# Kernel tuning notes

Hardware: AMD Instinct MI355X
Metric: run time of the kernel (lower is better)

## Reference

```python
import jax, jax.numpy as jnp
import numpy as np

N_QUBITS = 10
DIM = 2 ** N_QUBITS  # 1024

# PennyLane QFT (wire 0 = MSB): QFT|x> = (1/sqrt(N)) sum_y exp(2*pi*i*x*y/N)|y>
_idx = np.arange(DIM)
QFT_MAT = jnp.asarray(np.exp(2j * np.pi * np.outer(_idx, _idx) / DIM) / np.sqrt(DIM), dtype=jnp.complex64)


def _rx(t):
    c = jnp.cos(0.5 * t).astype(jnp.complex64)
    s = jnp.sin(0.5 * t).astype(jnp.complex64)
    return jnp.stack([jnp.stack([c, -1j * s]), jnp.stack([-1j * s, c])])


def _ry(t):
    c = jnp.cos(0.5 * t).astype(jnp.complex64)
    s = jnp.sin(0.5 * t).astype(jnp.complex64)
    return jnp.stack([jnp.stack([c, -s]), jnp.stack([s, c])])


def _rz(t):
    e = jnp.exp(-0.5j * t.astype(jnp.complex64))
    z = jnp.zeros((), jnp.complex64)
    return jnp.stack([jnp.stack([e, z]), jnp.stack([z, jnp.conj(e)])])


def _apply_1q(state, U, q):
    # state: (B,) + (2,)*N_QUBITS; contract qubit axis q+1 with 2x2 gate U
    s = jnp.tensordot(U, state, axes=[[1], [q + 1]])  # new qubit axis moves to front
    return jnp.moveaxis(s, 0, q + 1)


def _apply_cnot(state, c, t):
    # flip target-qubit axis on the control=1 slice
    s0 = jax.lax.index_in_dim(state, 0, c + 1, keepdims=True)
    s1 = jax.lax.index_in_dim(state, 1, c + 1, keepdims=True)
    s1 = jnp.flip(s1, axis=t + 1)
    return jnp.concatenate([s0, s1], axis=c + 1)


def _forward(x, weights):
    B = x.shape[0]
    pad = DIM - x.shape[-1]
    xp = jnp.pad(x, ((0, 0), (0, pad))) if pad > 0 else x[..., :DIM]
    nrm = jnp.maximum(jnp.linalg.norm(xp, axis=-1, keepdims=True), 1e-8)
    state = (xp / nrm).astype(jnp.complex64).reshape((B,) + (2,) * N_QUBITS)

    for q in range(N_QUBITS):
        state = _apply_1q(state, _rx(weights[q, 0]), q)
    for q in range(N_QUBITS):
        state = _apply_1q(state, _ry(weights[q, 1]), q)
    for q in range(N_QUBITS):
        state = _apply_1q(state, _rz(weights[q, 2]), q)
    for q in range(N_QUBITS):  # ring entanglement
        state = _apply_cnot(state, q, (q + 1) % N_QUBITS)
    for q in range(N_QUBITS):
        state = _apply_1q(state, _ry(weights[q, 3]), q)

    # QFT over all wires as one dense matmul on the flattened statevector
    state = (state.reshape(B, DIM) @ QFT_MAT.T).reshape((B,) + (2,) * N_QUBITS)

    ex, ey, ez = [], [], []
    for q in range(N_QUBITS):
        a = jax.lax.index_in_dim(state, 0, q + 1, keepdims=False)
        b = jax.lax.index_in_dim(state, 1, q + 1, keepdims=False)
        axes = tuple(range(1, a.ndim))
        zab = jnp.sum(jnp.conj(a) * b, axis=axes)  # (B,)
        ex.append(2.0 * jnp.real(zab))             # <X_q>
        ey.append(2.0 * jnp.imag(zab))             # <Y_q>
        ez.append(jnp.sum(jnp.real(jnp.conj(a) * a - jnp.conj(b) * b), axis=axes))  # <Z_q>
    return jnp.stack(ex + ey + ez, axis=1).astype(jnp.float32)  # (B, 3*N_QUBITS)


def setup_inputs() -> dict:
    key = jax.random.key(0)
    k1, k2 = jax.random.split(key)
    x = jax.random.normal(k1, (8192, 768), dtype=jnp.float32)
    weights = jax.random.normal(k2, (N_QUBITS, 4), dtype=jnp.float32) * 0.01
    return {"x": x, "weights": weights}


def reference(x, weights):
    return _forward(x, weights)
```

## Files before the change

### kernel.cpp

```cpp
#include <hip/hip_runtime.h>
#include <math.h>

#define NFEAT 768
#define NT    256

typedef float f2 __attribute__((ext_vector_type(2)));

__device__ __forceinline__ int swz(int j){ return j ^ (j >> 4) ^ ((j >> 2) & 0xC); }

__device__ __forceinline__ int cnot_perm(int j){
  int i = j;
  i ^= ((i >> 0) & 1) << 9;
  i ^= ((i >> 1) & 1) << 0;
  i ^= ((i >> 2) & 1) << 1;
  i ^= ((i >> 3) & 1) << 2;
  i ^= ((i >> 4) & 1) << 3;
  i ^= ((i >> 5) & 1) << 4;
  i ^= ((i >> 6) & 1) << 5;
  i ^= ((i >> 7) & 1) << 6;
  i ^= ((i >> 8) & 1) << 7;
  i ^= ((i >> 9) & 1) << 8;
  return i;
}

template<int CTRL>
__device__ __forceinline__ float dpp_mov(float x){
  return __builtin_bit_cast(float,
    __builtin_amdgcn_update_dpp(0, __builtin_bit_cast(int, x), CTRL, 0xF, 0xF, true));
}
template<int CTRL>
__device__ __forceinline__ float dpp_add(float x){ return x + dpp_mov<CTRL>(x); }

__device__ __forceinline__ f2 pk_cmul(f2 s, f2 v){
  f2 d;
  asm("v_pk_mul_f32 %0, %1, %2 op_sel:[0,0] op_sel_hi:[0,1]\n\t"
      "v_pk_fma_f32 %0, %1, %2, %0 op_sel:[1,1,0] op_sel_hi:[1,0,1] neg_lo:[0,1,0]"
      : "=&v"(d) : "v"(s), "v"(v));
  return d;
}
__device__ __forceinline__ f2 pk_cfma(f2 s, f2 v, f2 acc){
  f2 d;
  asm("v_pk_fma_f32 %0, %2, %3, %1 op_sel:[0,0,0] op_sel_hi:[0,1,1]\n\t"
      "v_pk_fma_f32 %0, %2, %3, %0 op_sel:[1,1,0] op_sel_hi:[1,0,1] neg_lo:[0,1,0]"
      : "=&v"(d) : "v"(acc), "v"(s), "v"(v));
  return d;
}
__device__ __forceinline__ f2 pk_cross(f2 a, f2 b, f2 acc){
  f2 d;
  asm("v_pk_fma_f32 %0, %2, %3, %1 op_sel:[0,1,0] op_sel_hi:[1,0,1] neg_hi:[1,0,0]"
      : "=&v"(d) : "v"(acc), "v"(a), "v"(b));
  return d;
}
__device__ __forceinline__ void pk_ry(f2 cs, f2& a, f2& b){
  f2 t1, t2, na, nb;
  asm("v_pk_mul_f32 %0, %2, %3 op_sel:[1,0] op_sel_hi:[1,1] neg_lo:[1,0] neg_hi:[1,0]\n\t"
      "v_pk_mul_f32 %1, %2, %4 op_sel:[1,0] op_sel_hi:[1,1]"
      : "=&v"(t1), "=&v"(t2) : "v"(cs), "v"(b), "v"(a));
  asm("v_pk_fma_f32 %0, %2, %3, %4 op_sel:[0,0,0] op_sel_hi:[0,1,1]\n\t"
      "v_pk_fma_f32 %1, %2, %5, %6 op_sel:[0,0,0] op_sel_hi:[0,1,1]"
      : "=&v"(na), "=&v"(nb) : "v"(cs), "v"(a), "v"(t1), "v"(b), "v"(t2));
  a = na; b = nb;
}
__device__ __forceinline__ void gateU(const f2* g, f2& a, f2& b){
  const f2 na = pk_cfma(g[1], b, pk_cmul(g[0], a));
  const f2 nb = pk_cfma(g[3], b, pk_cmul(g[2], a));
  a = na; b = nb;
}
__device__ __forceinline__ void bfly(f2& a, f2& b, f2 tw){
  const f2 u = a + b, v = a - b;
  a = u; b = pk_cmul(tw, v);
}
__device__ __forceinline__ void bfly1(f2& a, f2& b){
  const f2 u = a + b, v = a - b; a = u; b = v;
}
__device__ __forceinline__ void bflyI(f2& a, f2& b){
  const f2 u = a + b, v = a - b; a = u; b = f2{-v.y, v.x};
}

template<int MASK>
__device__ __forceinline__ void gate_on(f2* xv, const f2* g){
  #pragma unroll
  for (int m = 0; m < 16; ++m) if (!(m & MASK)) gateU(g, xv[m], xv[m|MASK]);
}
template<int MASK>
__device__ __forceinline__ void ry_on(f2* xv, const f2 cs){
  #pragma unroll
  for (int m = 0; m < 16; ++m) if (!(m & MASK)) pk_ry(cs, xv[m], xv[m|MASK]);
}

template<int SH>
__device__ __forceinline__ void rd16(const f2* bb, int a0, f2* xv){
  #pragma unroll
  for (int m = 0; m < 16; ++m) xv[m] = bb[a0 ^ swz(m << SH)];
}
template<int SH>
__device__ __forceinline__ void wr16(f2* bb, int a0, const f2* xv){
  #pragma unroll
  for (int m = 0; m < 16; ++m) bb[a0 ^ swz(m << SH)] = xv[m];
}

__device__ __forceinline__ void fft16(f2* xv, const f2 BT){
  const f2 T64c  = { 0.9238795325112867f, 0.3826834323650898f };
  const f2 T128c = { 0.7071067811865476f, 0.7071067811865476f };
  const f2 tB = pk_cmul(BT, BT);
  const f2 tC = pk_cmul(tB, tB);
  const f2 tD = pk_cmul(tC, tC);
  { f2 tw = BT;
    bfly(xv[0], xv[8], tw);
    #pragma unroll
    for (int m = 1; m < 8; ++m){ tw = pk_cmul(tw, T64c); bfly(xv[m], xv[m+8], tw); } }
  { f2 tw = tB;
    bfly(xv[0], xv[4], tw); bfly(xv[8], xv[12], tw);
    #pragma unroll
    for (int k = 1; k < 4; ++k){ tw = pk_cmul(tw, T128c); bfly(xv[k], xv[k+4], tw); bfly(xv[8+k], xv[12+k], tw); } }
  { const f2 itC = {-tC.y, tC.x};
    #pragma unroll
    for (int m = 0; m < 16; ++m) if (!(m & 2)) bfly(xv[m], xv[m|2], (m & 1) ? itC : tC); }
  #pragma unroll
  for (int m = 0; m < 16; m += 2) bfly(xv[m], xv[m+1], tD);
}

template<int MASK>
__device__ __forceinline__ f2 pairsum16(const f2* z){
  f2 rp = {0.f, 0.f}, ip = {0.f, 0.f};
  #pragma unroll
  for (int m = 0; m < 16; ++m) if (!(m & MASK)){
    rp = z[m]*z[m|MASK] + rp;
    ip = pk_cross(z[m], z[m|MASK], ip);
  }
  return f2{ rp.x + rp.y, ip.x + ip.y };
}

__global__ void gate_prep(const float* __restrict__ w, float* __restrict__ gt){
  const int t = threadIdx.x;
  if (t >= 10) return;
  const float ha = 0.5f*w[t*4+0], hb = 0.5f*w[t*4+1];
  const float hg = 0.5f*w[t*4+2], hd = 0.5f*w[t*4+3];
  const float ca = cosf(ha), sa = sinf(ha);
  const float cb = cosf(hb), sb = sinf(hb);
  const float cg = cosf(hg), sg = sinf(hg);
  const float m00r = cb*ca, m00i =  sb*sa;
  const float m01r = -sb*ca, m01i = -cb*sa;
  const float m10r =  sb*ca, m10i = -cb*sa;
  const float m11r = cb*ca,  m11i = -sb*sa;
  gt[8*t+0] = cg*m00r + sg*m00i;  gt[8*t+1] = cg*m00i - sg*m00r;
  gt[8*t+2] = cg*m01r + sg*m01i;  gt[8*t+3] = cg*m01i - sg*m01r;
  gt[8*t+4] = cg*m10r - sg*m10i;  gt[8*t+5] = cg*m10i + sg*m10r;
  gt[8*t+6] = cg*m11r - sg*m11i;  gt[8*t+7] = cg*m11i + sg*m11r;
  gt[80+2*t] = cosf(hd); gt[81+2*t] = sinf(hd);
}

__global__ void __launch_bounds__(NT)
qqk_kernel(const float* __restrict__ x, const float* __restrict__ gt,
           float* __restrict__ out)
{
  __shared__ f2 smem[4*1024];
  const int t = threadIdx.x, wave = t >> 6, lane = t & 63;
  f2* bb = smem + (wave << 10);
  const f2* g2  = (const f2*)gt;
  const f2* gry = (const f2*)(gt + 80);
  const size_t e = (size_t)blockIdx.x * 4 + wave;
  const float* xg = x + e * NFEAT;

  const int aA = swz(lane);
  const int aB = swz(((lane >> 2) << 6) | (lane & 3));
  const int aC = swz(lane << 4);

  f2 xv[16];
  float ss = 0.f;
  #pragma unroll
  for (int m = 0; m < 12; ++m){ const float v = xg[(m << 6) + lane]; xv[m] = f2{v, 0.f}; ss += v*v; }
  #pragma unroll
  for (int m = 12; m < 16; ++m) xv[m] = f2{0.f, 0.f};
  ss = dpp_add<0xB1>(ss); ss = dpp_add<0x4E>(ss);
  ss += __shfl_xor(ss, 4); ss += __shfl_xor(ss, 8); ss += __shfl_xor(ss, 16); ss += __shfl_xor(ss, 32);
  const float invn = 1.0f / fmaxf(sqrtf(ss), 1e-8f);
  #pragma unroll
  for (int m = 0; m < 12; ++m) xv[m].x *= invn;
  gate_on<8>(xv, g2+0); gate_on<4>(xv, g2+4); gate_on<2>(xv, g2+8); gate_on<1>(xv, g2+12);
  wr16<6>(bb, aA, xv);
  rd16<2>(bb, aB, xv);
  gate_on<8>(xv, g2+16); gate_on<4>(xv, g2+20); gate_on<2>(xv, g2+24); gate_on<1>(xv, g2+28);
  wr16<2>(bb, aB, xv);
  rd16<0>(bb, aC, xv);
  gate_on<2>(xv, g2+32); gate_on<1>(xv, g2+36);
  wr16<0>(bb, aC, xv);
  { const int ag = swz(cnot_perm(lane));
    #pragma unroll
    for (int m = 0; m < 16; ++m) xv[m] = bb[ag ^ swz(cnot_perm(m << 6))];
  }
  ry_on<8>(xv, gry[0]); ry_on<4>(xv, gry[1]); ry_on<2>(xv, gry[2]); ry_on<1>(xv, gry[3]);
  wr16<6>(bb, aA, xv);
  rd16<2>(bb, aB, xv);
  ry_on<8>(xv, gry[4]); ry_on<4>(xv, gry[5]); ry_on<2>(xv, gry[6]); ry_on<1>(xv, gry[7]);
  wr16<2>(bb, aB, xv);
  rd16<0>(bb, aC, xv);
  ry_on<2>(xv, gry[8]); ry_on<1>(xv, gry[9]);
  wr16<0>(bb, aC, xv);
  rd16<6>(bb, aA, xv);
  { float sa, ca; __sincosf((float)lane * 6.135923151542565e-3f, &sa, &ca);
    fft16(xv, f2{ca, sa}); }
  wr16<6>(bb, aA, xv);
  rd16<2>(bb, aB, xv);
  { float sa, ca; __sincosf((float)(lane & 3) * 9.817477042468104e-2f, &sa, &ca);
    fft16(xv, f2{ca, sa}); }
  wr16<2>(bb, aB, xv);
  rd16<0>(bb, aC, xv);
  #pragma unroll
  for (int m = 0; m < 16; ++m) if (!(m & 2)){ if (m & 1) bflyI(xv[m], xv[m|2]); else bfly1(xv[m], xv[m|2]); }
  #pragma unroll
  for (int m = 0; m < 16; m += 2) bfly1(xv[m], xv[m+1]);
  wr16<0>(bb, aC, xv);
  f2 xrxi[10];
  xrxi[0] = pairsum16<1>(xv); xrxi[1] = pairsum16<2>(xv);
  xrxi[2] = pairsum16<4>(xv); xrxi[3] = pairsum16<8>(xv);
  float S = 0.f, z0 = 0.f, z1 = 0.f, z2 = 0.f, z3 = 0.f;
  #pragma unroll
  for (int m = 0; m < 16; ++m){
    const f2 q = xv[m]*xv[m]; const float n = q.x + q.y;
    S += n;
    z0 += (m & 1) ? -n : n;  z1 += (m & 2) ? -n : n;
    z2 += (m & 4) ? -n : n;  z3 += (m & 8) ? -n : n;
  }
  rd16<6>(bb, aA, xv);
  xrxi[6] = pairsum16<1>(xv); xrxi[7] = pairsum16<2>(xv);
  xrxi[8] = pairsum16<4>(xv); xrxi[9] = pairsum16<8>(xv);
  rd16<2>(bb, aB, xv);
  xrxi[4] = pairsum16<4>(xv); xrxi[5] = pairsum16<8>(xv);

  float d0, d1, d2, d3, d4, d5;
  { float s = S, wv;
    wv = dpp_mov<0xB1>(s); d0 = (lane & 1)  ? (wv - s) : (s - wv); s += wv;
    wv = dpp_mov<0x4E>(s); d1 = (lane & 2)  ? (wv - s) : (s - wv); s += wv;
    wv = __shfl_xor(s, 4);  d2 = (lane & 4)  ? (wv - s) : (s - wv); s += wv;
    wv = __shfl_xor(s, 8);  d3 = (lane & 8)  ? (wv - s) : (s - wv); s += wv;
    wv = __shfl_xor(s, 16); d4 = (lane & 16) ? (wv - s) : (s - wv); s += wv;
    wv = __shfl_xor(s, 32); d5 = (lane & 32) ? (wv - s) : (s - wv); s += wv;
    d0 = dpp_add<0x4E>(d0); d0 += __shfl_xor(d0, 4); d0 += __shfl_xor(d0, 8); d0 += __shfl_xor(d0, 16); d0 += __shfl_xor(d0, 32);
    d1 += __shfl_xor(d1, 4); d1 += __shfl_xor(d1, 8); d1 += __shfl_xor(d1, 16); d1 += __shfl_xor(d1, 32);
    d2 += __shfl_xor(d2, 8); d2 += __shfl_xor(d2, 16); d2 += __shfl_xor(d2, 32);
    d3 += __shfl_xor(d3, 16); d3 += __shfl_xor(d3, 32);
    d4 += __shfl_xor(d4, 32);
  }

  #pragma unroll
  for (int q = 0; q < 10; ++q){
    xrxi[q].x = dpp_add<0x4E>(dpp_add<0xB1>(xrxi[q].x));
    xrxi[q].y = dpp_add<0x4E>(dpp_add<0xB1>(xrxi[q].y));
  }
  z0 = dpp_add<0x4E>(dpp_add<0xB1>(z0));
  z1 = dpp_add<0x4E>(dpp_add<0xB1>(z1));
  z2 = dpp_add<0x4E>(dpp_add<0xB1>(z2));
  z3 = dpp_add<0x4E>(dpp_add<0xB1>(z3));
  float* rb = (float*)bb;
  const int g = lane >> 2;
  if ((lane & 3) == 0){
    #pragma unroll
    for (int q = 0; q < 10; ++q){ rb[q*16 + g] = xrxi[q].x; rb[(10+q)*16 + g] = xrxi[q].y; }
    rb[20*16 + g] = z0; rb[21*16 + g] = z1; rb[22*16 + g] = z2; rb[23*16 + g] = z3;
  }
  float* ob = out + e * 30;
  if (lane < 24){
    float acc = 0.f;
    #pragma unroll
    for (int gg = 0; gg < 16; ++gg) acc += rb[lane*16 + gg];
    ob[lane] = acc * ((lane < 20) ? (2.0f/1024.0f) : (1.0f/1024.0f));
  }
  if (lane == 0){
    const float zs = 1.0f/1024.0f;
    ob[24] = d0*zs; ob[25] = d1*zs; ob[26] = d2*zs;
    ob[27] = d3*zs; ob[28] = d4*zs; ob[29] = d5*zs;
  }
}

extern "C" void kernel_launch(void* const* d_in, const int* in_sizes, int n_in,
                              void* d_out, int out_size, void* d_ws, size_t ws_size,
                              hipStream_t stream) {
  const float* x = (const float*)d_in[0];
  const float* w = (const float*)d_in[1];
  float* out = (float*)d_out;
  float* gt  = (float*)d_ws;
  const int B = in_sizes[0] / NFEAT;
  gate_prep<<<1, 16, 0, stream>>>(w, gt);
  qqk_kernel<<<B/4, NT, 0, stream>>>(x, gt, out);
}
```

Baseline: 47.53 us.

## Remap statevector LDS layout for 128-bit vectorized shared-memory transposes

Reassigns qubits so that each lane holds adjacent amplitude pairs, which lets every LDS transpose use float4 loads and stores instead of scalar f2 accesses, with a new XOR swizzle. The global input load also becomes float2. The gate schedule and FFT stages are rewritten for the new mapping: one 8-point radix split per stage with precomputed twiddle constants. Compiler memory fences are added between shared-memory phases, and the new layout risks bank conflicts or indexing errors.

New measurement: 45.61 us. 4.0% less time.

```diff
diff --git a/kernel.cpp b/kernel.cpp
--- a/kernel.cpp
+++ b/kernel.cpp
@@ -5,8 +5,9 @@
 #define NT    256
 
 typedef float f2 __attribute__((ext_vector_type(2)));
-
-__device__ __forceinline__ int swz(int j){ return j ^ (j >> 4) ^ ((j >> 2) & 0xC); }
+#define MEMFENCE() asm volatile("" ::: "memory")
+
+__device__ __forceinline__ int swz2(int j){ return j ^ ((j >> 3) & 0xE); }
 
 __device__ __forceinline__ int cnot_perm(int j){
   int i = j;
@@ -66,6 +67,7 @@
   const f2 nb = pk_cfma(g[3], b, pk_cmul(g[2], a));
   a = na; b = nb;
 }
+__device__ __forceinline__ f2 rot90(f2 v){ return f2{-v.y, v.x}; }
 __device__ __forceinline__ void bfly(f2& a, f2& b, f2 tw){
   const f2 u = a + b, v = a - b;
   a = u; b = pk_cmul(tw, v);
@@ -87,39 +89,6 @@
   #pragma unroll
   for (int m = 0; m < 16; ++m) if (!(m & MASK)) pk_ry(cs, xv[m], xv[m|MASK]);
 }
-
-template<int SH>
-__device__ __forceinline__ void rd16(const f2* bb, int a0, f2* xv){
-  #pragma unroll
-  for (int m = 0; m < 16; ++m) xv[m] = bb[a0 ^ swz(m << SH)];
-}
-template<int SH>
-__device__ __forceinline__ void wr16(f2* bb, int a0, const f2* xv){
-  #pragma unroll
-  for (int m = 0; m < 16; ++m) bb[a0 ^ swz(m << SH)] = xv[m];
-}
-
-__device__ __forceinline__ void fft16(f2* xv, const f2 BT){
-  const f2 T64c  = { 0.9238795325112867f, 0.3826834323650898f };
-  const f2 T128c = { 0.7071067811865476f, 0.7071067811865476f };
-  const f2 tB = pk_cmul(BT, BT);
-  const f2 tC = pk_cmul(tB, tB);
-  const f2 tD = pk_cmul(tC, tC);
-  { f2 tw = BT;
-    bfly(xv[0], xv[8], tw);
-    #pragma unroll
-    for (int m = 1; m < 8; ++m){ tw = pk_cmul(tw, T64c); bfly(xv[m], xv[m+8], tw); } }
-  { f2 tw = tB;
-    bfly(xv[0], xv[4], tw); bfly(xv[8], xv[12], tw);
-    #pragma unroll
-    for (int k = 1; k < 4; ++k){ tw = pk_cmul(tw, T128c); bfly(xv[k], xv[k+4], tw); bfly(xv[8+k], xv[12+k], tw); } }
-  { const f2 itC = {-tC.y, tC.x};
-    #pragma unroll
-    for (int m = 0; m < 16; ++m) if (!(m & 2)) bfly(xv[m], xv[m|2], (m & 1) ? itC : tC); }
-  #pragma unroll
-  for (int m = 0; m < 16; m += 2) bfly(xv[m], xv[m+1], tD);
-}
-
 template<int MASK>
 __device__ __forceinline__ f2 pairsum16(const f2* z){
   f2 rp = {0.f, 0.f}, ip = {0.f, 0.f};
@@ -129,6 +98,43 @@
     ip = pk_cross(z[m], z[m|MASK], ip);
   }
   return f2{ rp.x + rp.y, ip.x + ip.y };
+}
+
+__device__ __forceinline__ void rdA(const f2* bb, int a0, f2* xv){
+  #pragma unroll
+  for (int k = 0; k < 8; ++k){
+    const float4 v = *(const float4*)(bb + (a0 ^ (k << 7)));
+    xv[2*k] = f2{v.x, v.y}; xv[2*k+1] = f2{v.z, v.w};
+  }
+}
+__device__ __forceinline__ void wrA(f2* bb, int a0, const f2* xv){
+  #pragma unroll
+  for (int k = 0; k < 8; ++k)
+    *(float4*)(bb + (a0 ^ (k << 7))) = make_float4(xv[2*k].x, xv[2*k].y, xv[2*k+1].x, xv[2*k+1].y);
+}
+__device__ __forceinline__ void rdB(const f2* bb, int a0, f2* xv){
+  #pragma unroll
+  for (int k = 0; k < 8; ++k){
+    const float4 v = *(const float4*)(bb + (a0 ^ ((k << 4) | (k << 1))));
+    xv[2*k] = f2{v.x, v.y}; xv[2*k+1] = f2{v.z, v.w};
+  }
+}
+__device__ __forceinline__ void wrB(f2* bb, int a0, const f2* xv){
+  #pragma unroll
+  for (int k = 0; k < 8; ++k)
+    *(float4*)(bb + (a0 ^ ((k << 4) | (k << 1)))) = make_float4(xv[2*k].x, xv[2*k].y, xv[2*k+1].x, xv[2*k+1].y);
+}
+__device__ __forceinline__ void rdC(const f2* bb, int a0, f2* xv){
+  #pragma unroll
+  for (int k = 0; k < 8; ++k){
+    const float4 v = *(const float4*)(bb + (a0 ^ (k << 1)));
+    xv[2*k] = f2{v.x, v.y}; xv[2*k+1] = f2{v.z, v.w};
+  }
+}
+__device__ __forceinline__ void wrC(f2* bb, int a0, const f2* xv){
+  #pragma unroll
+  for (int k = 0; k < 8; ++k)
+    *(float4*)(bb + (a0 ^ (k << 1))) = make_float4(xv[2*k].x, xv[2*k].y, xv[2*k+1].x, xv[2*k+1].y);
 }
 
 __global__ void gate_prep(const float* __restrict__ w, float* __restrict__ gt){
@@ -154,7 +160,7 @@
 qqk_kernel(const float* __restrict__ x, const float* __restrict__ gt,
            float* __restrict__ out)
 {
-  __shared__ f2 smem[4*1024];
+  __shared__ __align__(16) f2 smem[4096];
   const int t = threadIdx.x, wave = t >> 6, lane = t & 63;
   f2* bb = smem + (wave << 10);
   const f2* g2  = (const f2*)gt;
@@ -162,14 +168,28 @@
   const size_t e = (size_t)blockIdx.x * 4 + wave;
   const float* xg = x + e * NFEAT;
 
-  const int aA = swz(lane);
-  const int aB = swz(((lane >> 2) << 6) | (lane & 3));
-  const int aC = swz(lane << 4);
+  const int aA = (lane << 1) ^ ((lane >> 2) & 14);
+  const int aB = ((lane >> 3) << 7) | ((lane & 7) << 1);
+  const int aC = (lane << 4) ^ ((lane << 1) & 14);
+
+  const f2 T1c   = { 0.9999811752826011f, 0.0061358846491545f };
+  const f2 T2c   = { 0.9999247018391445f, 0.0122715382857199f };
+  const f2 T4c   = { 0.9996988186962042f, 0.0245412285229123f };
+  const f2 T8c   = { 0.9987954562051724f, 0.0490676743274180f };
+  const f2 T16c  = { 0.9951847266721969f, 0.0980171403295606f };
+  const f2 T32c  = { 0.9807852804032304f, 0.1950903220161283f };
+  const float c45 = 0.7071067811865476f, c22 = 0.9238795325112867f, s22 = 0.3826834323650898f;
+  const f2 T64c  = { c22, s22 };
+  const f2 T128c = { c45, c45 };
 
   f2 xv[16];
   float ss = 0.f;
   #pragma unroll
-  for (int m = 0; m < 12; ++m){ const float v = xg[(m << 6) + lane]; xv[m] = f2{v, 0.f}; ss += v*v; }
+  for (int k = 0; k < 6; ++k){
+    const float2 v = *(const float2*)(xg + (k << 7) + (lane << 1));
+    xv[2*k] = f2{v.x, 0.f}; xv[2*k+1] = f2{v.y, 0.f};
+    ss += v.x*v.x + v.y*v.y;
+  }
   #pragma unroll
   for (int m = 12; m < 16; ++m) xv[m] = f2{0.f, 0.f};
   ss = dpp_add<0xB1>(ss); ss = dpp_add<0x4E>(ss);
@@ -177,40 +197,98 @@
   const float invn = 1.0f / fmaxf(sqrtf(ss), 1e-8f);
   #pragma unroll
   for (int m = 0; m < 12; ++m) xv[m].x *= invn;
-  gate_on<8>(xv, g2+0); gate_on<4>(xv, g2+4); gate_on<2>(xv, g2+8); gate_on<1>(xv, g2+12);
-  wr16<6>(bb, aA, xv);
-  rd16<2>(bb, aB, xv);
-  gate_on<8>(xv, g2+16); gate_on<4>(xv, g2+20); gate_on<2>(xv, g2+24); gate_on<1>(xv, g2+28);
-  wr16<2>(bb, aB, xv);
-  rd16<0>(bb, aC, xv);
-  gate_on<2>(xv, g2+32); gate_on<1>(xv, g2+36);
-  wr16<0>(bb, aC, xv);
-  { const int ag = swz(cnot_perm(lane));
-    #pragma unroll
-    for (int m = 0; m < 16; ++m) xv[m] = bb[ag ^ swz(cnot_perm(m << 6))];
-  }
-  ry_on<8>(xv, gry[0]); ry_on<4>(xv, gry[1]); ry_on<2>(xv, gry[2]); ry_on<1>(xv, gry[3]);
-  wr16<6>(bb, aA, xv);
-  rd16<2>(bb, aB, xv);
-  ry_on<8>(xv, gry[4]); ry_on<4>(xv, gry[5]); ry_on<2>(xv, gry[6]); ry_on<1>(xv, gry[7]);
-  wr16<2>(bb, aB, xv);
-  rd16<0>(bb, aC, xv);
-  ry_on<2>(xv, gry[8]); ry_on<1>(xv, gry[9]);
-  wr16<0>(bb, aC, xv);
-  rd16<6>(bb, aA, xv);
-  { float sa, ca; __sincosf((float)lane * 6.135923151542565e-3f, &sa, &ca);
-    fft16(xv, f2{ca, sa}); }
-  wr16<6>(bb, aA, xv);
-  rd16<2>(bb, aB, xv);
-  { float sa, ca; __sincosf((float)(lane & 3) * 9.817477042468104e-2f, &sa, &ca);
-    fft16(xv, f2{ca, sa}); }
-  wr16<2>(bb, aB, xv);
-  rd16<0>(bb, aC, xv);
-  #pragma unroll
-  for (int m = 0; m < 16; ++m) if (!(m & 2)){ if (m & 1) bflyI(xv[m], xv[m|2]); else bfly1(xv[m], xv[m|2]); }
+  gate_on<8>(xv, g2+0); gate_on<4>(xv, g2+4); gate_on<2>(xv, g2+8); gate_on<1>(xv, g2+36);
+  wrA(bb, aA, xv);
+  MEMFENCE();
+  rdB(bb, aB, xv);
+  gate_on<8>(xv, g2+12); gate_on<4>(xv, g2+16); gate_on<2>(xv, g2+20);
+  wrB(bb, aB, xv);
+  MEMFENCE();
+  rdC(bb, aC, xv);
+  gate_on<8>(xv, g2+24); gate_on<4>(xv, g2+28); gate_on<2>(xv, g2+32);
+  wrC(bb, aC, xv);
+  MEMFENCE();
+  { const int ag = swz2(cnot_perm(lane << 4));
+    #pragma unroll
+    for (int m = 0; m < 16; ++m) xv[m] = bb[ag ^ swz2(cnot_perm(m))];
+  }
+  MEMFENCE();
+  ry_on<8>(xv, gry[6]); ry_on<4>(xv, gry[7]); ry_on<2>(xv, gry[8]); ry_on<1>(xv, gry[9]);
+  wrC(bb, aC, xv);
+  MEMFENCE();
+  rdB(bb, aB, xv);
+  ry_on<8>(xv, gry[3]); ry_on<4>(xv, gry[4]); ry_on<2>(xv, gry[5]);
+  wrB(bb, aB, xv);
+  MEMFENCE();
+  rdA(bb, aA, xv);
+  ry_on<8>(xv, gry[0]); ry_on<4>(xv, gry[1]); ry_on<2>(xv, gry[2]);
+  { float sa, ca; __sincosf((float)lane * 1.2271846303085130e-2f, &sa, &ca);
+    const f2 BT = {ca, sa};
+    const f2 BT2 = pk_cmul(BT, BT);
+    const f2 BT4 = pk_cmul(BT2, BT2);
+    f2 t9[8];
+    t9[0] = BT;               t9[1] = pk_cmul(BT, T1c);
+    t9[2] = pk_cmul(BT, T128c); t9[3] = pk_cmul(t9[1], T128c);
+    t9[4] = rot90(t9[0]); t9[5] = rot90(t9[1]); t9[6] = rot90(t9[2]); t9[7] = rot90(t9[3]);
+    #pragma unroll
+    for (int m = 0; m < 8; ++m) bfly(xv[m], xv[m+8], t9[m]);
+    f2 u[4];
+    u[0] = BT2; u[1] = pk_cmul(BT2, T2c); u[2] = rot90(u[0]); u[3] = rot90(u[1]);
+    #pragma unroll
+    for (int m = 0; m < 16; ++m) if (!(m & 4)) bfly(xv[m], xv[m|4], u[m & 3]);
+    f2 v2[2];
+    v2[0] = BT4; v2[1] = pk_cmul(BT4, T4c);
+    #pragma unroll
+    for (int m = 0; m < 16; ++m) if (!(m & 2)) bfly(xv[m], xv[m|2], v2[m & 1]);
+  }
+  wrA(bb, aA, xv);
+  MEMFENCE();
+  rdB(bb, aB, xv);
+  { float sa, ca; __sincosf((float)(lane & 7) * 9.8174770424681035e-2f, &sa, &ca);
+    const f2 CT = {ca, sa};
+    const f2 CT2 = pk_cmul(CT, CT);
+    const f2 CT4 = pk_cmul(CT2, CT2);
+    f2 t6[8];
+    t6[0] = CT;               t6[1] = pk_cmul(CT, T8c);
+    t6[2] = pk_cmul(CT, T128c); t6[3] = pk_cmul(t6[1], T128c);
+    t6[4] = rot90(t6[0]); t6[5] = rot90(t6[1]); t6[6] = rot90(t6[2]); t6[7] = rot90(t6[3]);
+    #pragma unroll
+    for (int m = 0; m < 8; ++m) bfly(xv[m], xv[m+8], t6[m]);
+    f2 u[4];
+    u[0] = CT2; u[1] = pk_cmul(CT2, T16c); u[2] = rot90(u[0]); u[3] = rot90(u[1]);
+    #pragma unroll
+    for (int m = 0; m < 16; ++m) if (!(m & 4)) bfly(xv[m], xv[m|4], u[m & 3]);
+    f2 v2[2];
+    v2[0] = CT4; v2[1] = pk_cmul(CT4, T32c);
+    #pragma unroll
+    for (int m = 0; m < 16; ++m) if (!(m & 2)) bfly(xv[m], xv[m|2], v2[m & 1]);
+  }
+  wrB(bb, aB, xv);
+  MEMFENCE();
+  rdC(bb, aC, xv);
+  bfly1(xv[0], xv[8]);
+  bfly (xv[1], xv[9],  T64c);
+  bfly (xv[2], xv[10], T128c);
+  bfly (xv[3], xv[11], f2{ s22, c22});
+  bflyI(xv[4], xv[12]);
+  bfly (xv[5], xv[13], f2{-s22, c22});
+  bfly (xv[6], xv[14], f2{-c45, c45});
+  bfly (xv[7], xv[15], f2{-c22, s22});
+  #pragma unroll
+  for (int m = 0; m < 16; ++m) if (!(m & 4)){
+    const int s = m & 3;
+    if      (s == 0) bfly1(xv[m], xv[m|4]);
+    else if (s == 1) bfly (xv[m], xv[m|4], T128c);
+    else if (s == 2) bflyI(xv[m], xv[m|4]);
+    else             bfly (xv[m], xv[m|4], f2{-c45, c45});
+  }
+  #pragma unroll
+  for (int m = 0; m < 16; ++m) if (!(m & 2)){
+    if (m & 1) bflyI(xv[m], xv[m|2]); else bfly1(xv[m], xv[m|2]);
+  }
   #pragma unroll
   for (int m = 0; m < 16; m += 2) bfly1(xv[m], xv[m+1]);
-  wr16<0>(bb, aC, xv);
+  wrC(bb, aC, xv);
   f2 xrxi[10];
   xrxi[0] = pairsum16<1>(xv); xrxi[1] = pairsum16<2>(xv);
   xrxi[2] = pairsum16<4>(xv); xrxi[3] = pairsum16<8>(xv);
@@ -222,11 +300,12 @@
     z0 += (m & 1) ? -n : n;  z1 += (m & 2) ? -n : n;
     z2 += (m & 4) ? -n : n;  z3 += (m & 8) ? -n : n;
   }
-  rd16<6>(bb, aA, xv);
-  xrxi[6] = pairsum16<1>(xv); xrxi[7] = pairsum16<2>(xv);
-  xrxi[8] = pairsum16<4>(xv); xrxi[9] = pairsum16<8>(xv);
-  rd16<2>(bb, aB, xv);
-  xrxi[4] = pairsum16<4>(xv); xrxi[5] = pairsum16<8>(xv);
+  MEMFENCE();
+  rdA(bb, aA, xv);
+  xrxi[9] = pairsum16<8>(xv); xrxi[8] = pairsum16<4>(xv); xrxi[7] = pairsum16<2>(xv);
+  rdB(bb, aB, xv);
+  xrxi[6] = pairsum16<8>(xv); xrxi[5] = pairsum16<4>(xv); xrxi[4] = pairsum16<2>(xv);
+  MEMFENCE();
 
   float d0, d1, d2, d3, d4, d5;
   { float s = S, wv;
@@ -259,6 +338,7 @@
     for (int q = 0; q < 10; ++q){ rb[q*16 + g] = xrxi[q].x; rb[(10+q)*16 + g] = xrxi[q].y; }
     rb[20*16 + g] = z0; rb[21*16 + g] = z1; rb[22*16 + g] = z2; rb[23*16 + g] = z3;
   }
+  MEMFENCE();
   float* ob = out + e * 30;
   if (lane < 24){
     float acc = 0.f;
```
